# Kernel tuning notes

Measured on AMD Instinct MI355X. Metric: run time of the kernel, lower is better.

The kernel has to match this reference:

```python
import jax, jax.numpy as jnp
import numpy as np

B, S, H, NH = 2, 2048, 2048, 16
HD = H // NH  # 128
NEG = -1e9


def setup_inputs() -> dict:
    key = jax.random.key(0)
    ks = jax.random.split(key, 5)
    hidden_states = jax.random.normal(ks[0], (B, S, H), dtype=jnp.float32)
    causal = jnp.tril(jnp.ones((S, S), dtype=bool))
    attention_mask = jnp.where(causal, 0.0, NEG).astype(jnp.float32)[None, None, :, :]
    scale = 0.02
    Wq = jax.random.normal(ks[1], (H, H), dtype=jnp.float32) * scale
    Wk = jax.random.normal(ks[2], (H, H), dtype=jnp.float32) * scale
    Wv = jax.random.normal(ks[3], (H, H), dtype=jnp.float32) * scale
    Wo = jax.random.normal(ks[4], (H, H), dtype=jnp.float32) * scale
    return {"hidden_states": hidden_states, "attention_mask": attention_mask,
            "Wq": Wq, "Wk": Wk, "Wv": Wv, "Wo": Wo}


def reference(hidden_states, attention_mask, Wq, Wk, Wv, Wo):
    # nn.Linear(bias=False): y = x @ W.T
    q = hidden_states @ Wq.T  # [B,S,H]
    k = hidden_states @ Wk.T
    v = hidden_states @ Wv.T
    # [B,S,NH,HD] -> [B,NH,S,HD]
    q = q.reshape(B, S, NH, HD).transpose(0, 2, 1, 3)
    k = k.reshape(B, S, NH, HD).transpose(0, 2, 1, 3)
    v = v.reshape(B, S, NH, HD).transpose(0, 2, 1, 3)
    scaling = HD ** -0.5
    # [B,NH,S,S]
    scores = jnp.einsum('bhqd,bhkd->bhqk', q, k) * scaling + attention_mask
    attn = jax.nn.softmax(scores.astype(jnp.float32), axis=-1).astype(q.dtype)
    out = jnp.einsum('bhqk,bhkd->bhqd', attn, v)  # [B,NH,S,HD]
    out = out.transpose(0, 2, 1, 3).reshape(B, S, H)
    return out @ Wo.T
```

## Files before the change

### kernel.cpp

```cpp
#include <hip/hip_runtime.h>

typedef unsigned short u16;
typedef __bf16 bf16x8 __attribute__((ext_vector_type(8)));
typedef float floatx4 __attribute__((ext_vector_type(4)));

#define B_ 2
#define S_ 2048
#define H_ 2048
#define NH_ 16
#define BS_ 4096
#define QKSTR 4096
#define PSTR 72

#define SCL_Q (0.08838834764831843f * 1.4426950408889634f)

#define PART_CH 4194304
#define LP_CH 32768

__device__ __forceinline__ u16 f2bf(float f) {
  unsigned u = __float_as_uint(f);
  u += 0x7fffu + ((u >> 16) & 1u);
  return (u16)(u >> 16);
}

__device__ __forceinline__ void gl_lds16(const void* g, void* l) {
  __builtin_amdgcn_global_load_lds((__attribute__((address_space(1))) void*)g,
                                   (__attribute__((address_space(3))) void*)l,
                                   16, 0, 0);
}

__device__ __forceinline__ floatx4 mfma16(bf16x8 a, bf16x8 b, floatx4 c) {
  return __builtin_amdgcn_mfma_f32_16x16x32_bf16(a, b, c, 0, 0, 0);
}

__global__ void cast_all(const float* __restrict__ X, const float* __restrict__ Wq,
                         const float* __restrict__ Wk, const float* __restrict__ Wv,
                         const float* __restrict__ Wo, u16* __restrict__ Xb,
                         u16* __restrict__ Wb) {
  const int XG = (BS_ * H_) / 4;
  const int WG = (H_ * H_) / 4;
  int i = blockIdx.x * 256 + threadIdx.x;
  const float* src;
  u16* dst;
  int j;
  if (i < XG) {
    src = X; dst = Xb; j = i;
  } else {
    int t = i - XG;
    int w = t >> 20;
    j = t & (WG - 1);
    src = (w == 0) ? Wq : (w == 1) ? Wk : (w == 2) ? Wv : Wo;
    dst = Wb + (size_t)w * (H_ * (size_t)H_);
  }
  float4 v = ((const float4*)src)[j];
  ushort4 o;
  o.x = f2bf(v.x); o.y = f2bf(v.y); o.z = f2bf(v.z); o.w = f2bf(v.w);
  ((ushort4*)dst)[j] = o;
}

template <bool F32OUT>
__global__ __launch_bounds__(256, 2)
void gemm_bt(const u16* __restrict__ A, const u16* __restrict__ Bm,
             void* __restrict__ Cp, int M, int N, int K, float scl, int ncut) {
  __shared__ __attribute__((aligned(16))) u16 lA[128 * 64];
  __shared__ __attribute__((aligned(16))) u16 lB[128 * 64];
  const int tid = threadIdx.x;
  const int wave = tid >> 6, lane = tid & 63;
  const int bm = blockIdx.y * 128, bn = blockIdx.x * 128;
  const int wm = (wave >> 1) * 64, wn = (wave & 1) * 64;
  const int laneRow = lane & 15, laneQ = lane >> 4;
  const int rs = laneRow & 7;

  floatx4 acc[4][4] = {};

  const int sr = tid >> 3;
  const int sc = (((tid & 7) ^ ((tid >> 3) & 7)) * 8);
  const u16* Ap = A + (size_t)(bm + sr) * K + sc;
  const u16* Bp = Bm + (size_t)(bn + sr) * K + sc;
  char* lAc = (char*)lA + wave * 1024;
  char* lBc = (char*)lB + wave * 1024;

  for (int k0 = 0; k0 < K; k0 += 64) {
    __syncthreads();
#pragma unroll
    for (int i = 0; i < 4; ++i) {
      gl_lds16(Ap + (size_t)i * 32 * K + k0, lAc + i * 4096);
      gl_lds16(Bp + (size_t)i * 32 * K + k0, lBc + i * 4096);
    }
    __syncthreads();
#pragma unroll
    for (int ks = 0; ks < 2; ++ks) {
      bf16x8 af[4], bf[4];
#pragma unroll
      for (int t = 0; t < 4; ++t)
        af[t] = *(const bf16x8*)&lA[(wm + t * 16 + laneRow) * 64 +
                                    (((ks * 4 + laneQ) ^ rs) * 8)];
#pragma unroll
      for (int t = 0; t < 4; ++t)
        bf[t] = *(const bf16x8*)&lB[(wn + t * 16 + laneRow) * 64 +
                                    (((ks * 4 + laneQ) ^ rs) * 8)];
#pragma unroll
      for (int mt = 0; mt < 4; ++mt)
#pragma unroll
        for (int nt = 0; nt < 4; ++nt)
          acc[mt][nt] = mfma16(af[mt], bf[nt], acc[mt][nt]);
    }
  }
#pragma unroll
  for (int mt = 0; mt < 4; ++mt)
#pragma unroll
    for (int nt = 0; nt < 4; ++nt)
#pragma unroll
      for (int r = 0; r < 4; ++r) {
        int m = bm + wm + mt * 16 + laneQ * 4 + r;
        int n = bn + wn + nt * 16 + laneRow;
        if (F32OUT) {
          ((float*)Cp)[(size_t)m * N + n] = acc[mt][nt][r];
        } else {
          float s = (n < ncut) ? scl : 1.0f;
          ((u16*)Cp)[(size_t)m * N + n] = f2bf(acc[mt][nt][r] * s);
        }
      }
}

__global__ __launch_bounds__(256, 3)
void flash_attn(const u16* __restrict__ QKg, const u16* __restrict__ Vt,
                u16* __restrict__ Og, float* __restrict__ Part,
                float* __restrict__ Lp) {
  __shared__ __attribute__((aligned(16))) u16 smem[64 * 128 + 128 * 64 + 128 * PSTR];
  u16* lK = smem;
  u16* lV = smem + 8192;
  u16* lP = smem + 16384;

  const int tid = threadIdx.x;
  const int wave = tid >> 6, lane = tid & 63;
  const int laneRow = lane & 15, laneQ = lane >> 4;
  const int rs = laneRow & 7;
  const int wq = wave * 32;
  const int bx = blockIdx.x, bh = blockIdx.y;
  const int b = bh >> 4, h = bh & 15;

  int qt, ktBeg, ktEnd, ch;
  if (bx < 16) {
    qt = 15 - (bx >> 1);
    ch = bx & 1;
    ktBeg = ch * (qt + 1);
    ktEnd = ktBeg + (qt + 1);
  } else {
    qt = 23 - bx;
    ch = 0;
    ktBeg = 0;
    ktEnd = 2 * (qt + 1);
  }
  const bool partial = (bx < 16);

  const int c16 = (((tid & 15) ^ ((tid >> 4) & 7)) * 8);
  const int c8s = (((tid & 7) ^ ((tid >> 3) & 7)) * 8);

  {
    const int r = tid >> 4;
    const u16* Qp = QKg + (size_t)(b * S_ + qt * 128 + r) * QKSTR + h * 128 + c16;
    char* ld = (char*)smem + wave * 1024;
#pragma unroll
    for (int i = 0; i < 8; ++i)
      gl_lds16(Qp + (size_t)i * 16 * QKSTR, ld + i * 4096);
  }
  __syncthreads();
  bf16x8 qf[2][4];
#pragma unroll
  for (int mt = 0; mt < 2; ++mt)
#pragma unroll
    for (int ks = 0; ks < 4; ++ks)
      qf[mt][ks] = *(const bf16x8*)&smem[(wq + mt * 16 + laneRow) * 128 +
                                         (((ks * 4 + laneQ) ^ rs) * 8)];

  floatx4 accO[2][8] = {};
  float ps[2][4] = {};

  for (int kt = ktBeg; kt < ktEnd; ++kt) {
    __syncthreads();
    {
      const int r = tid >> 4;
      const u16* Kp = QKg + 2048 + (size_t)(b * S_ + kt * 64 + r) * QKSTR + h * 128 + c16;
      char* ld = (char*)lK + wave * 1024;
#pragma unroll
      for (int i = 0; i < 4; ++i)
        gl_lds16(Kp + (size_t)i * 16 * QKSTR, ld + i * 4096);
    }
    {
      const int r = tid >> 3;
      const u16* Vp = Vt + (size_t)(h * 128 + r) * BS_ + b * S_ + kt * 64 + c8s;
      char* ld = (char*)lV + wave * 1024;
#pragma unroll
      for (int i = 0; i < 4; ++i)
        gl_lds16(Vp + (size_t)i * 32 * BS_, ld + i * 4096);
    }
    __syncthreads();

    floatx4 accS[2][4] = {};
#pragma unroll
    for (int ks = 0; ks < 4; ++ks) {
      bf16x8 kf[4];
#pragma unroll
      for (int nt = 0; nt < 4; ++nt)
        kf[nt] = *(const bf16x8*)&lK[(nt * 16 + laneRow) * 128 +
                                     (((ks * 4 + laneQ) ^ rs) * 8)];
#pragma unroll
      for (int mt = 0; mt < 2; ++mt)
#pragma unroll
        for (int nt = 0; nt < 4; ++nt)
          accS[mt][nt] = mfma16(qf[mt][ks], kf[nt], accS[mt][nt]);
    }
    if (kt * 64 + 63 > qt * 128 + wq) {
#pragma unroll
      for (int mt = 0; mt < 2; ++mt)
#pragma unroll
        for (int r = 0; r < 4; ++r) {
          int q = qt * 128 + wq + mt * 16 + laneQ * 4 + r;
#pragma unroll
          for (int nt = 0; nt < 4; ++nt) {
            int k = kt * 64 + nt * 16 + laneRow;
            if (k > q) accS[mt][nt][r] = -1e30f;
          }
        }
    }

#pragma unroll
    for (int mt = 0; mt < 2; ++mt)
#pragma unroll
      for (int r = 0; r < 4; ++r) {
#pragma unroll
        for (int nt = 0; nt < 4; ++nt) {
          float p = exp2f(accS[mt][nt][r]);
          accS[mt][nt][r] = p;
          ps[mt][r] += p;
        }
      }
#pragma unroll
    for (int mt = 0; mt < 2; ++mt)
#pragma unroll
      for (int nt = 0; nt < 4; ++nt)
#pragma unroll
        for (int r = 0; r < 4; ++r)
          lP[(wq + mt * 16 + laneQ * 4 + r) * PSTR + nt * 16 + laneRow] =
              f2bf(accS[mt][nt][r]);

#pragma unroll
    for (int ks = 0; ks < 2; ++ks) {
      bf16x8 pf[2], vf[8];
#pragma unroll
      for (int mt = 0; mt < 2; ++mt)
        pf[mt] = *(const bf16x8*)&lP[(wq + mt * 16 + laneRow) * PSTR + ks * 32 + laneQ * 8];
#pragma unroll
      for (int nt = 0; nt < 8; ++nt)
        vf[nt] = *(const bf16x8*)&lV[(nt * 16 + laneRow) * 64 +
                                     (((ks * 4 + laneQ) ^ rs) * 8)];
#pragma unroll
      for (int mt = 0; mt < 2; ++mt)
#pragma unroll
        for (int nt = 0; nt < 8; ++nt)
          accO[mt][nt] = mfma16(pf[mt], vf[nt], accO[mt][nt]);
    }
  }

  float li[2][4];
#pragma unroll
  for (int mt = 0; mt < 2; ++mt)
#pragma unroll
    for (int r = 0; r < 4; ++r) {
      float l = ps[mt][r];
#pragma unroll
      for (int off = 1; off < 16; off <<= 1)
        l += __shfl_xor(l, off);
      li[mt][r] = l;
    }

  if (!partial) {
#pragma unroll
    for (int mt = 0; mt < 2; ++mt)
#pragma unroll
      for (int r = 0; r < 4; ++r) {
        float inv = 1.0f / li[mt][r];
        int m = qt * 128 + wq + mt * 16 + laneQ * 4 + r;
#pragma unroll
        for (int nt = 0; nt < 8; ++nt) {
          int n = nt * 16 + laneRow;
          Og[(size_t)(b * S_ + m) * H_ + h * 128 + n] = f2bf(accO[mt][nt][r] * inv);
        }
      }
  } else {
    float* P0 = Part + (size_t)ch * PART_CH;
    float* L0 = Lp + (size_t)ch * LP_CH;
#pragma unroll
    for (int mt = 0; mt < 2; ++mt)
#pragma unroll
      for (int r = 0; r < 4; ++r) {
        int qrow = wq + mt * 16 + laneQ * 4 + r;
        int pIdx = ((qt - 8) * 32 + bh) * 128 + qrow;
        if (laneRow == 0) L0[pIdx] = li[mt][r];
#pragma unroll
        for (int nt = 0; nt < 8; ++nt)
          P0[(size_t)pIdx * 128 + nt * 16 + laneRow] = accO[mt][nt][r];
      }
  }
}

__global__ void combine(const float* __restrict__ Part, const float* __restrict__ Lp,
                        u16* __restrict__ Og) {
  int j = blockIdx.x * 256 + threadIdx.x;
  int e = j * 4;
  int d = e & 127;
  int rowid = e >> 7;
  float4 a = ((const float4*)Part)[j];
  float4 c = ((const float4*)(Part + PART_CH))[j];
  float inv = 1.0f / (Lp[rowid] + Lp[LP_CH + rowid]);
  int q = rowid & 127;
  int bh = (rowid >> 7) & 31;
  int qt = 8 + (rowid >> 12);
  int b = bh >> 4, h = bh & 15;
  int m = qt * 128 + q;
  ushort4 o;
  o.x = f2bf((a.x + c.x) * inv);
  o.y = f2bf((a.y + c.y) * inv);
  o.z = f2bf((a.z + c.z) * inv);
  o.w = f2bf((a.w + c.w) * inv);
  *(ushort4*)&Og[(size_t)(b * S_ + m) * H_ + h * 128 + d] = o;
}

extern "C" void kernel_launch(void* const* d_in, const int* in_sizes, int n_in,
                              void* d_out, int out_size, void* d_ws, size_t ws_size,
                              hipStream_t stream) {
  const float* X  = (const float*)d_in[0];
  const float* Wq = (const float*)d_in[2];
  const float* Wk = (const float*)d_in[3];
  const float* Wv = (const float*)d_in[4];
  const float* Wo = (const float*)d_in[5];

  char* ws = (char*)d_ws;
  u16* Xb  = (u16*)(ws);
  u16* Wqb = (u16*)(ws + (16u << 20));
  u16* Wvb = Wqb + 2 * (size_t)H_ * H_;
  u16* Wob = Wqb + 3 * (size_t)H_ * H_;
  u16* QKb = (u16*)(ws + (48u << 20));
  u16* Vtb = (u16*)(ws + (80u << 20));
  u16* AOb = (u16*)(ws + (96u << 20));
  float* Part = (float*)ws;
  float* Lp   = (float*)(ws + 2u * PART_CH * sizeof(float));

  {
    int groups = (BS_ * H_) / 4 + H_ * H_;
    cast_all<<<groups / 256, 256, 0, stream>>>(X, Wq, Wk, Wv, Wo, Xb, Wqb);
  }

  gemm_bt<false><<<dim3(32, 32), 256, 0, stream>>>(Xb, Wqb, QKb, BS_, 4096, H_, SCL_Q, 2048);
  gemm_bt<false><<<dim3(32, 16), 256, 0, stream>>>(Wvb, Xb, Vtb, H_, BS_, H_, 1.0f, 0);

  flash_attn<<<dim3(24, B_ * NH_), 256, 0, stream>>>(QKb, Vtb, AOb, Part, Lp);
  combine<<<PART_CH / 4 / 256, 256, 0, stream>>>(Part, Lp, AOb);

  gemm_bt<true><<<dim3(16, 32), 256, 0, stream>>>(AOb, Wob, (float*)d_out, BS_, H_, H_, 1.0f, 0);
}
```

Baseline: 399.3 us.

## Prefetch next K tile during softmax, reorder block schedule, add MFMA priority

The next K tile's global-to-LDS load is now issued after the score MFMAs and softmax, so it overlaps with the P·V stage. The per-iteration barrier structure is reorganised to match, and the first K tile is preloaded before the loop. The mapping from block index to (q-tile, chunk, partial) moves into a lookup table that reorders block launch. s_setprio raises wave priority around the MFMA loops. The reduced barriers depend on the V load completing before the later barrier, which is a synchronisation risk.

```diff
diff --git a/kernel.cpp b/kernel.cpp
--- a/kernel.cpp
+++ b/kernel.cpp
@@ -140,19 +140,17 @@
   const int bx = blockIdx.x, bh = blockIdx.y;
   const int b = bh >> 4, h = bh & 15;
 
-  int qt, ktBeg, ktEnd, ch;
-  if (bx < 16) {
-    qt = 15 - (bx >> 1);
-    ch = bx & 1;
-    ktBeg = ch * (qt + 1);
-    ktEnd = ktBeg + (qt + 1);
-  } else {
-    qt = 23 - bx;
-    ch = 0;
-    ktBeg = 0;
-    ktEnd = 2 * (qt + 1);
-  }
-  const bool partial = (bx < 16);
+  static const unsigned char tbl[24] = {
+      61, 28, 57, 59, 55, 24, 51, 47,
+      63, 53, 49, 41, 43, 37, 45, 20,
+      0,  4,  8,  12, 33, 39, 35, 16};
+  const int enc = tbl[bx];
+  const int qt = enc >> 2;
+  const int ch = (enc >> 1) & 1;
+  const bool partial = enc & 1;
+  const int nkt = qt + 1;
+  const int ktBeg = partial ? ch * nkt : 0;
+  const int ktEnd = partial ? ktBeg + nkt : 2 * nkt;
 
   const int c16 = (((tid & 15) ^ ((tid >> 4) & 7)) * 8);
   const int c8s = (((tid & 7) ^ ((tid >> 3) & 7)) * 8);
@@ -173,20 +171,22 @@
     for (int ks = 0; ks < 4; ++ks)
       qf[mt][ks] = *(const bf16x8*)&smem[(wq + mt * 16 + laneRow) * 128 +
                                          (((ks * 4 + laneQ) ^ rs) * 8)];
+  __syncthreads();
+
+  {
+    const int r = tid >> 4;
+    const u16* Kp = QKg + 2048 + (size_t)(b * S_ + ktBeg * 64 + r) * QKSTR + h * 128 + c16;
+    char* ld = (char*)lK + wave * 1024;
+#pragma unroll
+    for (int i = 0; i < 4; ++i)
+      gl_lds16(Kp + (size_t)i * 16 * QKSTR, ld + i * 4096);
+  }
+  __syncthreads();
 
   floatx4 accO[2][8] = {};
   float ps[2][4] = {};
 
   for (int kt = ktBeg; kt < ktEnd; ++kt) {
-    __syncthreads();
-    {
-      const int r = tid >> 4;
-      const u16* Kp = QKg + 2048 + (size_t)(b * S_ + kt * 64 + r) * QKSTR + h * 128 + c16;
-      char* ld = (char*)lK + wave * 1024;
-#pragma unroll
-      for (int i = 0; i < 4; ++i)
-        gl_lds16(Kp + (size_t)i * 16 * QKSTR, ld + i * 4096);
-    }
     {
       const int r = tid >> 3;
       const u16* Vp = Vt + (size_t)(h * 128 + r) * BS_ + b * S_ + kt * 64 + c8s;
@@ -195,9 +195,9 @@
       for (int i = 0; i < 4; ++i)
         gl_lds16(Vp + (size_t)i * 32 * BS_, ld + i * 4096);
     }
-    __syncthreads();
 
     floatx4 accS[2][4] = {};
+    __builtin_amdgcn_s_setprio(1);
 #pragma unroll
     for (int ks = 0; ks < 4; ++ks) {
       bf16x8 kf[4];
@@ -211,6 +211,8 @@
         for (int nt = 0; nt < 4; ++nt)
           accS[mt][nt] = mfma16(qf[mt][ks], kf[nt], accS[mt][nt]);
     }
+    __builtin_amdgcn_s_setprio(0);
+
     if (kt * 64 + 63 > qt * 128 + wq) {
 #pragma unroll
       for (int mt = 0; mt < 2; ++mt)
@@ -236,6 +238,18 @@
           ps[mt][r] += p;
         }
       }
+
+    __syncthreads();
+
+    if (kt + 1 < ktEnd) {
+      const int r = tid >> 4;
+      const u16* Kp = QKg + 2048 + (size_t)(b * S_ + (kt + 1) * 64 + r) * QKSTR + h * 128 + c16;
+      char* ld = (char*)lK + wave * 1024;
+#pragma unroll
+      for (int i = 0; i < 4; ++i)
+        gl_lds16(Kp + (size_t)i * 16 * QKSTR, ld + i * 4096);
+    }
+
 #pragma unroll
     for (int mt = 0; mt < 2; ++mt)
 #pragma unroll
@@ -245,6 +259,7 @@
           lP[(wq + mt * 16 + laneQ * 4 + r) * PSTR + nt * 16 + laneRow] =
               f2bf(accS[mt][nt][r]);
 
+    __builtin_amdgcn_s_setprio(1);
 #pragma unroll
     for (int ks = 0; ks < 2; ++ks) {
       bf16x8 pf[2], vf[8];
@@ -261,6 +276,9 @@
         for (int nt = 0; nt < 8; ++nt)
           accO[mt][nt] = mfma16(pf[mt], vf[nt], accO[mt][nt]);
     }
+    __builtin_amdgcn_s_setprio(0);
+
+    __syncthreads();
   }
 
   float li[2][4];
```

Measured after the change: 425.8 us. 6.6% more time.

## Replace GEMMs with double-buffered 256x256 tile kernel and merge QK/V launches

Applied to the files above, without the earlier changes.

The 128x128 single-buffered GEMM is replaced by a 512-thread 256x256 tile core. It double-buffers the LDS K-slices so the next tile's loads overlap the current tile's MFMAs, and raises priority around the MFMA block. The QK and V projections now run in one launch of 384 blocks, and the output projection uses the same core. Larger tiles reuse more data per load, but they need 128 KB of LDS per block, use more registers, and leave fewer blocks for the output GEMM (128 blocks on a part with many CUs), so occupancy and wave tails may suffer.

```diff
diff --git a/kernel.cpp b/kernel.cpp
--- a/kernel.cpp
+++ b/kernel.cpp
@@ -59,55 +59,90 @@
 }
 
 template <bool F32OUT>
-__global__ __launch_bounds__(256, 2)
-void gemm_bt(const u16* __restrict__ A, const u16* __restrict__ Bm,
-             void* __restrict__ Cp, int M, int N, int K, float scl, int ncut) {
-  __shared__ __attribute__((aligned(16))) u16 lA[128 * 64];
-  __shared__ __attribute__((aligned(16))) u16 lB[128 * 64];
+__device__ __forceinline__ void gemm256_core(
+    const u16* __restrict__ A, const u16* __restrict__ Bm, void* __restrict__ Cp,
+    int N, int K, float scl, int ncut, int bm, int bn,
+    u16* lA, u16* lB) {
   const int tid = threadIdx.x;
   const int wave = tid >> 6, lane = tid & 63;
-  const int bm = blockIdx.y * 128, bn = blockIdx.x * 128;
-  const int wm = (wave >> 1) * 64, wn = (wave & 1) * 64;
   const int laneRow = lane & 15, laneQ = lane >> 4;
   const int rs = laneRow & 7;
-
-  floatx4 acc[4][4] = {};
-
-  const int sr = tid >> 3;
-  const int sc = (((tid & 7) ^ ((tid >> 3) & 7)) * 8);
-  const u16* Ap = A + (size_t)(bm + sr) * K + sc;
-  const u16* Bp = Bm + (size_t)(bn + sr) * K + sc;
-  char* lAc = (char*)lA + wave * 1024;
-  char* lBc = (char*)lB + wave * 1024;
-
-  for (int k0 = 0; k0 < K; k0 += 64) {
-    __syncthreads();
-#pragma unroll
-    for (int i = 0; i < 4; ++i) {
-      gl_lds16(Ap + (size_t)i * 32 * K + k0, lAc + i * 4096);
-      gl_lds16(Bp + (size_t)i * 32 * K + k0, lBc + i * 4096);
-    }
-    __syncthreads();
-#pragma unroll
-    for (int ks = 0; ks < 2; ++ks) {
-      bf16x8 af[4], bf[4];
-#pragma unroll
-      for (int t = 0; t < 4; ++t)
-        af[t] = *(const bf16x8*)&lA[(wm + t * 16 + laneRow) * 64 +
-                                    (((ks * 4 + laneQ) ^ rs) * 8)];
-#pragma unroll
-      for (int t = 0; t < 4; ++t)
-        bf[t] = *(const bf16x8*)&lB[(wn + t * 16 + laneRow) * 64 +
-                                    (((ks * 4 + laneQ) ^ rs) * 8)];
+  const int wm = (wave >> 2) * 128;
+  const int wn = (wave & 3) * 64;
+
+  floatx4 acc[8][4] = {};
+
+  const int srow = lane >> 3;
+  const int sg = ((lane & 7) ^ (srow & 7)) * 8;
+  const u16* Abase = A + (size_t)(bm + wave * 16 + srow) * K + sg;
+  const u16* Bbase = Bm + (size_t)(bn + wave * 16 + srow) * K + sg;
+  u16* ldA = lA + wave * 1024;
+  u16* ldB = lB + wave * 1024;
+
+  const int NT = K >> 6;
+
+#pragma unroll
+  for (int hh = 0; hh < 2; ++hh) {
+    const u16* sa = Abase + (size_t)hh * 128 * K;
+    gl_lds16(sa, ldA + hh * 8192);
+    gl_lds16(sa + (size_t)8 * K, (char*)(ldA + hh * 8192) + 1024);
+    const u16* sb = Bbase + (size_t)hh * 128 * K;
+    gl_lds16(sb, ldB + hh * 8192);
+    gl_lds16(sb + (size_t)8 * K, (char*)(ldB + hh * 8192) + 1024);
+  }
+
+  for (int kt = 0; kt < NT; ++kt) {
+    const int cur = (kt & 1) * 16384;
+    asm volatile("s_waitcnt vmcnt(0)" ::: "memory");
+    asm volatile("s_barrier" ::: "memory");
+    if (kt + 1 < NT) {
+      const int nxt = 16384 - cur;
+      const size_t kc = (size_t)(kt + 1) * 64;
+#pragma unroll
+      for (int hh = 0; hh < 2; ++hh) {
+        const u16* sa = Abase + (size_t)hh * 128 * K + kc;
+        gl_lds16(sa, ldA + nxt + hh * 8192);
+        gl_lds16(sa + (size_t)8 * K, (char*)(ldA + nxt + hh * 8192) + 1024);
+      }
+#pragma unroll
+      for (int hh = 0; hh < 2; ++hh) {
+        const u16* sb = Bbase + (size_t)hh * 128 * K + kc;
+        gl_lds16(sb, ldB + nxt + hh * 8192);
+        gl_lds16(sb + (size_t)8 * K, (char*)(ldB + nxt + hh * 8192) + 1024);
+      }
+    }
+    __builtin_amdgcn_sched_barrier(0);
+
+    bf16x8 bfr[4][2];
+#pragma unroll
+    for (int nt = 0; nt < 4; ++nt)
+#pragma unroll
+      for (int ks = 0; ks < 2; ++ks)
+        bfr[nt][ks] = *(const bf16x8*)&lB[cur + (wn + nt * 16 + laneRow) * 64 +
+                                          ((ks * 4 + laneQ) ^ rs) * 8];
+    __builtin_amdgcn_s_setprio(1);
+#pragma unroll
+    for (int mh = 0; mh < 2; ++mh) {
+      bf16x8 afr[4][2];
 #pragma unroll
       for (int mt = 0; mt < 4; ++mt)
 #pragma unroll
+        for (int ks = 0; ks < 2; ++ks)
+          afr[mt][ks] = *(const bf16x8*)&lA[cur + (wm + mh * 64 + mt * 16 + laneRow) * 64 +
+                                            ((ks * 4 + laneQ) ^ rs) * 8];
+#pragma unroll
+      for (int mt = 0; mt < 4; ++mt)
+#pragma unroll
         for (int nt = 0; nt < 4; ++nt)
-          acc[mt][nt] = mfma16(af[mt], bf[nt], acc[mt][nt]);
-    }
-  }
-#pragma unroll
-  for (int mt = 0; mt < 4; ++mt)
+#pragma unroll
+          for (int ks = 0; ks < 2; ++ks)
+            acc[mh * 4 + mt][nt] = mfma16(afr[mt][ks], bfr[nt][ks], acc[mh * 4 + mt][nt]);
+    }
+    __builtin_amdgcn_s_setprio(0);
+  }
+
+#pragma unroll
+  for (int mt = 0; mt < 8; ++mt)
 #pragma unroll
     for (int nt = 0; nt < 4; ++nt)
 #pragma unroll
@@ -121,6 +156,33 @@
           ((u16*)Cp)[(size_t)m * N + n] = f2bf(acc[mt][nt][r] * s);
         }
       }
+}
+
+__global__ __launch_bounds__(512, 2)
+void gemm256_pair(const u16* __restrict__ Xb, const u16* __restrict__ Wqb,
+                  u16* __restrict__ QKb, const u16* __restrict__ Wvb,
+                  u16* __restrict__ Vtb) {
+  __shared__ __attribute__((aligned(16))) u16 lA[2][16384];
+  __shared__ __attribute__((aligned(16))) u16 lB[2][16384];
+  const int bid = blockIdx.x;
+  if (bid < 256) {
+    gemm256_core<false>(Xb, Wqb, QKb, 4096, 2048, SCL_Q, 2048,
+                        (bid >> 4) * 256, (bid & 15) * 256, &lA[0][0], &lB[0][0]);
+  } else {
+    const int t = bid - 256;
+    gemm256_core<false>(Wvb, Xb, Vtb, 4096, 2048, 1.0f, 0,
+                        (t >> 4) * 256, (t & 15) * 256, &lA[0][0], &lB[0][0]);
+  }
+}
+
+__global__ __launch_bounds__(512, 2)
+void gemm256_out(const u16* __restrict__ AOb, const u16* __restrict__ Wob,
+                 float* __restrict__ Out) {
+  __shared__ __attribute__((aligned(16))) u16 lA[2][16384];
+  __shared__ __attribute__((aligned(16))) u16 lB[2][16384];
+  gemm256_core<true>(AOb, Wob, Out, 2048, 2048, 1.0f, 0,
+                     (int)blockIdx.y * 256, (int)blockIdx.x * 256,
+                     &lA[0][0], &lB[0][0]);
 }
 
 __global__ __launch_bounds__(256, 3)
@@ -352,11 +414,10 @@
     cast_all<<<groups / 256, 256, 0, stream>>>(X, Wq, Wk, Wv, Wo, Xb, Wqb);
   }
 
-  gemm_bt<false><<<dim3(32, 32), 256, 0, stream>>>(Xb, Wqb, QKb, BS_, 4096, H_, SCL_Q, 2048);
-  gemm_bt<false><<<dim3(32, 16), 256, 0, stream>>>(Wvb, Xb, Vtb, H_, BS_, H_, 1.0f, 0);
+  gemm256_pair<<<dim3(384), 512, 0, stream>>>(Xb, Wqb, QKb, Wvb, Vtb);
 
   flash_attn<<<dim3(24, B_ * NH_), 256, 0, stream>>>(QKb, Vtb, AOb, Part, Lp);
   combine<<<PART_CH / 4 / 256, 256, 0, stream>>>(Part, Lp, AOb);
 
-  gemm_bt<true><<<dim3(16, 32), 256, 0, stream>>>(AOb, Wob, (float*)d_out, BS_, H_, H_, 1.0f, 0);
-}
+  gemm256_out<<<dim3(8, 16), 512, 0, stream>>>(AOb, Wob, (float*)d_out);
+}
```

After: 453.1 us. +13.5%, slower.

## Triple-buffer GEMM loads with 128x256 tiles and 512-thread blocks

Applied to the files above, without the earlier changes.

Replaces the single-buffered 128x128 GEMM with a 3-stage LDS ring buffer that prefetches two k-tiles ahead, using vmcnt waits and a single barrier per iteration. Tiles grow to 128x256 with 8 waves per block, and s_setprio is raised around the MFMA block. The aim is to overlap global-to-LDS traffic with matrix math and cut barrier stalls. It needs 144KB of LDS per block, which limits occupancy. Correctness also depends on the hand-counted vmcnt values.

```diff
diff --git a/kernel.cpp b/kernel.cpp
--- a/kernel.cpp
+++ b/kernel.cpp
@@ -59,53 +59,79 @@
 }
 
 template <bool F32OUT>
-__global__ __launch_bounds__(256, 2)
-void gemm_bt(const u16* __restrict__ A, const u16* __restrict__ Bm,
-             void* __restrict__ Cp, int M, int N, int K, float scl, int ncut) {
-  __shared__ __attribute__((aligned(16))) u16 lA[128 * 64];
-  __shared__ __attribute__((aligned(16))) u16 lB[128 * 64];
+__global__ __launch_bounds__(512, 2)
+void gemm3(const u16* __restrict__ A, const u16* __restrict__ Bm,
+           void* __restrict__ Cp, int N, int K, float scl, int ncut) {
+  __shared__ __attribute__((aligned(16))) u16 smem[3 * 24576];
   const int tid = threadIdx.x;
   const int wave = tid >> 6, lane = tid & 63;
-  const int bm = blockIdx.y * 128, bn = blockIdx.x * 128;
-  const int wm = (wave >> 1) * 64, wn = (wave & 1) * 64;
   const int laneRow = lane & 15, laneQ = lane >> 4;
   const int rs = laneRow & 7;
+  const int bm = blockIdx.y * 128, bn = blockIdx.x * 256;
+  const int wm = (wave >> 2) * 64;
+  const int wn = (wave & 3) * 64;
 
   floatx4 acc[4][4] = {};
 
-  const int sr = tid >> 3;
-  const int sc = (((tid & 7) ^ ((tid >> 3) & 7)) * 8);
-  const u16* Ap = A + (size_t)(bm + sr) * K + sc;
-  const u16* Bp = Bm + (size_t)(bn + sr) * K + sc;
-  char* lAc = (char*)lA + wave * 1024;
-  char* lBc = (char*)lB + wave * 1024;
-
-  for (int k0 = 0; k0 < K; k0 += 64) {
-    __syncthreads();
-#pragma unroll
-    for (int i = 0; i < 4; ++i) {
-      gl_lds16(Ap + (size_t)i * 32 * K + k0, lAc + i * 4096);
-      gl_lds16(Bp + (size_t)i * 32 * K + k0, lBc + i * 4096);
-    }
-    __syncthreads();
-#pragma unroll
-    for (int ks = 0; ks < 2; ++ks) {
-      bf16x8 af[4], bf[4];
-#pragma unroll
-      for (int t = 0; t < 4; ++t)
-        af[t] = *(const bf16x8*)&lA[(wm + t * 16 + laneRow) * 64 +
-                                    (((ks * 4 + laneQ) ^ rs) * 8)];
-#pragma unroll
-      for (int t = 0; t < 4; ++t)
-        bf[t] = *(const bf16x8*)&lB[(wn + t * 16 + laneRow) * 64 +
-                                    (((ks * 4 + laneQ) ^ rs) * 8)];
-#pragma unroll
-      for (int mt = 0; mt < 4; ++mt)
-#pragma unroll
-        for (int nt = 0; nt < 4; ++nt)
-          acc[mt][nt] = mfma16(af[mt], bf[nt], acc[mt][nt]);
-    }
-  }
+  const int srow = tid >> 3;
+  const int sg = (((tid & 7) ^ (srow & 7)) * 8);
+  const u16* Abase = A + (size_t)(bm + srow) * K + sg;
+  const u16* Bbase = Bm + (size_t)(bn + srow) * K + sg;
+  const int NT = K >> 6;
+
+  auto stage = [&](int buf, int kc) {
+    char* base = (char*)smem + buf * 49152 + wave * 1024;
+#pragma unroll
+    for (int i = 0; i < 2; ++i)
+      gl_lds16(Abase + (size_t)(i * 64) * K + kc, base + i * 8192);
+#pragma unroll
+    for (int j = 0; j < 4; ++j)
+      gl_lds16(Bbase + (size_t)(j * 64) * K + kc, base + 16384 + j * 8192);
+  };
+
+  stage(0, 0);
+  stage(1, 64);
+
+  int cur = 0;
+  for (int kt = 0; kt < NT; ++kt) {
+    if (kt < NT - 1)
+      asm volatile("s_waitcnt vmcnt(6)" ::: "memory");
+    else
+      asm volatile("s_waitcnt vmcnt(0)" ::: "memory");
+    asm volatile("s_barrier" ::: "memory");
+    if (kt + 2 < NT) {
+      int nb = cur + 2; if (nb >= 3) nb -= 3;
+      stage(nb, (kt + 2) << 6);
+    }
+    __builtin_amdgcn_sched_barrier(0);
+
+    const u16* bp = smem + cur * 24576;
+    bf16x8 af[4][2], bf[4][2];
+#pragma unroll
+    for (int mt = 0; mt < 4; ++mt)
+#pragma unroll
+      for (int ks = 0; ks < 2; ++ks)
+        af[mt][ks] = *(const bf16x8*)&bp[(wm + mt * 16 + laneRow) * 64 +
+                                         ((ks * 4 + laneQ) ^ rs) * 8];
+#pragma unroll
+    for (int nt = 0; nt < 4; ++nt)
+#pragma unroll
+      for (int ks = 0; ks < 2; ++ks)
+        bf[nt][ks] = *(const bf16x8*)&bp[8192 + (wn + nt * 16 + laneRow) * 64 +
+                                         ((ks * 4 + laneQ) ^ rs) * 8];
+    __builtin_amdgcn_s_setprio(1);
+#pragma unroll
+    for (int mt = 0; mt < 4; ++mt)
+#pragma unroll
+      for (int nt = 0; nt < 4; ++nt)
+#pragma unroll
+        for (int ks = 0; ks < 2; ++ks)
+          acc[mt][nt] = mfma16(af[mt][ks], bf[nt][ks], acc[mt][nt]);
+    __builtin_amdgcn_s_setprio(0);
+
+    cur += 1; if (cur == 3) cur = 0;
+  }
+
 #pragma unroll
   for (int mt = 0; mt < 4; ++mt)
 #pragma unroll
@@ -352,11 +378,11 @@
     cast_all<<<groups / 256, 256, 0, stream>>>(X, Wq, Wk, Wv, Wo, Xb, Wqb);
   }
 
-  gemm_bt<false><<<dim3(32, 32), 256, 0, stream>>>(Xb, Wqb, QKb, BS_, 4096, H_, SCL_Q, 2048);
-  gemm_bt<false><<<dim3(32, 16), 256, 0, stream>>>(Wvb, Xb, Vtb, H_, BS_, H_, 1.0f, 0);
+  gemm3<false><<<dim3(16, 32), 512, 0, stream>>>(Xb, Wqb, QKb, 4096, 2048, SCL_Q, 2048);
+  gemm3<false><<<dim3(16, 16), 512, 0, stream>>>(Wvb, Xb, Vtb, 4096, 2048, 1.0f, 0);
 
   flash_attn<<<dim3(24, B_ * NH_), 256, 0, stream>>>(QKb, Vtb, AOb, Part, Lp);
   combine<<<PART_CH / 4 / 256, 256, 0, stream>>>(Part, Lp, AOb);
 
-  gemm_bt<true><<<dim3(16, 32), 256, 0, stream>>>(AOb, Wob, (float*)d_out, BS_, H_, H_, 1.0f, 0);
-}
+  gemm3<true><<<dim3(8, 32), 512, 0, stream>>>(AOb, Wob, (float*)d_out, 2048, 2048, 1.0f, 0);
+}
```

Result: no change. 395.7 us (median of 2 runs) (-0.9%).
